# Kernel tuning notes

Measured on AMD Instinct MI355X. Metric: run time of the kernel, lower is better.

Reference implementation:

```python
import jax, jax.numpy as jnp
import numpy as np

N_GRAPHS = 64
NODES_PER_G = 640
N = N_GRAPHS * NODES_PER_G      # 40960 nodes
DEG = 16
E = N * DEG                     # 655360 edges
D = 128                         # hidden_dim == out_dim
POS = 16                        # pos_enc_dim
L = 4                           # n GatedGCN-LSPE layers
N_ATOM = 28
N_BOND = 4
EPS = 1e-6
BN_EPS = 1e-5


def _lin(x, w, b):
    return x @ w + b


def _bn(x, g, b):
    # torch BatchNorm1d training forward: biased batch stats
    m = x.mean(0)
    v = x.var(0)
    return (x - m) * jax.lax.rsqrt(v + BN_EPS) * g + b


def setup_inputs() -> dict:
    key = jax.random.key(0)
    ks = iter(jax.random.split(key, 64))
    def nrm(shape, s=0.1):
        return jax.random.normal(next(ks), shape, dtype=jnp.float32) * s
    h_atoms = jax.random.randint(next(ks), (N,), 0, N_ATOM)
    e_bonds = jax.random.randint(next(ks), (E,), 0, N_BOND)
    # keep edges within each graph of the batch
    epg = E // N_GRAPHS
    off = (jnp.arange(E) // epg) * NODES_PER_G
    src = jax.random.randint(next(ks), (E,), 0, NODES_PER_G) + off
    dst = jax.random.randint(next(ks), (E,), 0, NODES_PER_G) + off
    node_graph_ids = jnp.arange(N) // NODES_PER_G
    return dict(
        h_atoms=h_atoms, e_bonds=e_bonds, src=src, dst=dst,
        node_graph_ids=node_graph_ids,
        p=nrm((N, POS), 1.0),
        W_emb_h=nrm((N_ATOM, D)), W_emb_p=nrm((POS, D)), b_emb_p=nrm((D,)),
        W_emb_e=nrm((N_BOND, D)),
        A1_w=nrm((L, 2 * D, D)), A1_b=nrm((L, D)),
        A2_w=nrm((L, 2 * D, D)), A2_b=nrm((L, D)),
        B1_w=nrm((L, D, D)), B1_b=nrm((L, D)),
        B2_w=nrm((L, D, D)), B2_b=nrm((L, D)),
        B3_w=nrm((L, D, D)), B3_b=nrm((L, D)),
        C1_w=nrm((L, D, D)), C1_b=nrm((L, D)),
        C2_w=nrm((L, D, D)), C2_b=nrm((L, D)),
        bn_h_g=jnp.ones((L, D)), bn_h_b=jnp.zeros((L, D)),
        bn_e_g=jnp.ones((L, D)), bn_e_b=jnp.zeros((L, D)),
        p_out_w=nrm((D, POS)), p_out_b=nrm((POS,)),
        Whp_w=nrm((D + POS, D)), Whp_b=nrm((D,)),
        mlp_w0=nrm((D, D // 2)), mlp_b0=nrm((D // 2,)),
        mlp_w1=nrm((D // 2, D // 4)), mlp_b1=nrm((D // 4,)),
        mlp_w2=nrm((D // 4, 1)), mlp_b2=nrm((1,)),
    )


def _forward(p, W_emb_h, W_emb_p, b_emb_p, W_emb_e,
             A1_w, A1_b, A2_w, A2_b, B1_w, B1_b, B2_w, B2_b, B3_w, B3_b,
             C1_w, C1_b, C2_w, C2_b, bn_h_g, bn_h_b, bn_e_g, bn_e_b,
             p_out_w, p_out_b, Whp_w, Whp_b,
             mlp_w0, mlp_b0, mlp_w1, mlp_b1, mlp_w2, mlp_b2,
             h_atoms, e_bonds, src, dst, node_graph_ids):
    seg = lambda x, idx, n: jax.ops.segment_sum(x, idx, num_segments=n)
    h = W_emb_h[h_atoms]                      # [N,D] atom embedding
    pc = _lin(p, W_emb_p, b_emb_p)            # [N,D] PE embedding
    ef = W_emb_e[e_bonds]                     # [E,D] bond embedding
    for l in range(L):
        h_in, p_in, e_in = h, pc, ef
        # edge gates: hat_eta_ij = B1 h_i + B2 h_j + B3 e_ij (u=src, v=dst)
        hat_eta = (_lin(h, B1_w[l], B1_b[l])[src]
                   + _lin(h, B2_w[l], B2_b[l])[dst]
                   + _lin(ef, B3_w[l], B3_b[l]))          # [E,D]
        sig = jax.nn.sigmoid(hat_eta)
        eta = sig / (seg(sig, dst, N)[dst] + EPS)          # normalized gate
        hp = jnp.concatenate([h, pc], axis=-1)             # [N,2D]
        h_new = _lin(hp, A1_w[l], A1_b[l]) + seg(eta * _lin(hp, A2_w[l], A2_b[l])[src], dst, N)
        p_new = _lin(pc, C1_w[l], C1_b[l]) + seg(eta * _lin(pc, C2_w[l], C2_b[l])[src], dst, N)
        h_new = jax.nn.relu(_bn(h_new, bn_h_g[l], bn_h_b[l]))
        e_new = jax.nn.relu(_bn(hat_eta, bn_e_g[l], bn_e_b[l]))
        p_new = jnp.tanh(p_new)
        h = h_in + h_new       # residual (in_dim==out_dim)
        pc = p_in + p_new
        ef = e_in + e_new
    # pe_init == 'rand_walk' post-processing
    po = _lin(pc, p_out_w, p_out_b)                        # [N,POS]
    po = po - (seg(po, node_graph_ids, N_GRAPHS) / NODES_PER_G)[node_graph_ids]
    po = po / jnp.sqrt(seg(po * po, node_graph_ids, N_GRAPHS))[node_graph_ids]
    hp2 = _lin(jnp.concatenate([h, po], axis=-1), Whp_w, Whp_b)
    hg = seg(hp2, node_graph_ids, N_GRAPHS) / NODES_PER_G  # mean readout [G,D]
    y = jax.nn.relu(_lin(hg, mlp_w0, mlp_b0))
    y = jax.nn.relu(_lin(y, mlp_w1, mlp_b1))
    return _lin(y, mlp_w2, mlp_b2)                         # [G,1]


def reference(h_atoms, e_bonds, src, dst, node_graph_ids, p,
              W_emb_h, W_emb_p, b_emb_p, W_emb_e,
              A1_w, A1_b, A2_w, A2_b, B1_w, B1_b, B2_w, B2_b, B3_w, B3_b,
              C1_w, C1_b, C2_w, C2_b, bn_h_g, bn_h_b, bn_e_g, bn_e_b,
              p_out_w, p_out_b, Whp_w, Whp_b,
              mlp_w0, mlp_b0, mlp_w1, mlp_b1, mlp_w2, mlp_b2):
    return _forward(p, W_emb_h, W_emb_p, b_emb_p, W_emb_e,
                    A1_w, A1_b, A2_w, A2_b, B1_w, B1_b, B2_w, B2_b, B3_w, B3_b,
                    C1_w, C1_b, C2_w, C2_b, bn_h_g, bn_h_b, bn_e_g, bn_e_b,
                    p_out_w, p_out_b, Whp_w, Whp_b,
                    mlp_w0, mlp_b0, mlp_w1, mlp_b1, mlp_w2, mlp_b2,
                    h_atoms, e_bonds, src, dst, node_graph_ids)
```

## Files before the change

### kernel.cpp

```cpp
#include <hip/hip_runtime.h>
#include <math.h>

#define N_NODES 40960
#define N_EDGES 655360
#define NPG     640
#define NGRAPH  64
#define DH      128
#define NLAYERS 4
#define GATE_EPS 1e-6f
#define BN_EPS   1e-5f
#define ETPB    4

#define POOL_BYTES 580000000ull
__device__ __attribute__((aligned(256))) unsigned char g_pool[POOL_BYTES];

using short8  = __attribute__((ext_vector_type(8))) short;
using float4v = __attribute__((ext_vector_type(4))) float;

static __device__ __forceinline__ float sigmoidf_(float x) {
  return 1.f / (1.f + __expf(-x));
}
static __device__ __forceinline__ unsigned short f2bf(float f) {
  unsigned int u = __float_as_uint(f);
  unsigned int r = 0x7FFFu + ((u >> 16) & 1u);
  return (unsigned short)((u + r) >> 16);
}
static __device__ __forceinline__ float bf2f(unsigned short h) {
  return __uint_as_float(((unsigned int)h) << 16);
}

template <int WITH_STATS>
__global__ __launch_bounds__(256)
void egemm(const unsigned short* __restrict__ ef,
           const unsigned short* __restrict__ Wt,
           const float* __restrict__ bias,
           unsigned short* __restrict__ hat,
           const int* __restrict__ srcp, const int* __restrict__ dstp,
           const unsigned short* __restrict__ G1, const unsigned short* __restrict__ G2,
           float* __restrict__ stats, float* __restrict__ ssum)
{
  __shared__ unsigned short Ws[128][136];
  __shared__ float hatL[64][132];
  __shared__ int dstL[64];

  const int t    = threadIdx.x;
  const int w    = t >> 6;
  const int lane = t & 63;
  const int quad = lane >> 4;
  const int l16  = lane & 15;

#pragma unroll
  for (int i = 0; i < 8; ++i) {
    int flat = i * 256 + t;
    int n = flat >> 4, g = flat & 15;
    *reinterpret_cast<uint4*>(&Ws[n][g * 8]) =
        *reinterpret_cast<const uint4*>(&Wt[n * 128 + g * 8]);
  }
  __syncthreads();

  float stat_s = 0.f, stat_q = 0.f;

  for (int tile = 0; tile < ETPB; ++tile) {
    const size_t row0 = ((size_t)blockIdx.x * ETPB + tile) * 64;

    const size_t arow = row0 + w * 16 + l16;
    short8 a[4];
#pragma unroll
    for (int ks = 0; ks < 4; ++ks)
      a[ks] = *reinterpret_cast<const short8*>(&ef[arow * 128 + ks * 32 + quad * 8]);

    float4v acc[8];
#pragma unroll
    for (int j = 0; j < 8; ++j) acc[j] = (float4v){0.f, 0.f, 0.f, 0.f};
#pragma unroll
    for (int ks = 0; ks < 4; ++ks)
#pragma unroll
      for (int j = 0; j < 8; ++j) {
        short8 b = *reinterpret_cast<const short8*>(&Ws[j * 16 + l16][ks * 32 + quad * 8]);
        acc[j] = __builtin_amdgcn_mfma_f32_16x16x32_bf16(a[ks], b, acc[j], 0, 0, 0);
      }

    if (tile) __syncthreads();
#pragma unroll
    for (int j = 0; j < 8; ++j)
#pragma unroll
      for (int r = 0; r < 4; ++r)
        hatL[w * 16 + quad * 4 + r][j * 16 + l16] = acc[j][r];
    __syncthreads();

    {
      const int r = t >> 2, seg = t & 3;
      const size_t row = row0 + r;
      const int si = srcp[row], di = dstp[row];
      if (seg == 0) dstL[r] = di;
      const unsigned short* g1p = &G1[(size_t)si * 128];
      const unsigned short* g2p = &G2[(size_t)di * 128];
#pragma unroll
      for (int q2 = 0; q2 < 4; ++q2) {
        const int cc = seg * 32 + (((q2 + seg) & 3) << 3);
        float4 h0 = *reinterpret_cast<const float4*>(&hatL[r][cc]);
        float4 h1 = *reinterpret_cast<const float4*>(&hatL[r][cc + 4]);
        float4 b0 = *reinterpret_cast<const float4*>(&bias[cc]);
        float4 b1 = *reinterpret_cast<const float4*>(&bias[cc + 4]);
        uint4 g1 = *reinterpret_cast<const uint4*>(&g1p[cc]);
        uint4 g2 = *reinterpret_cast<const uint4*>(&g2p[cc]);
        float hv[8] = {h0.x, h0.y, h0.z, h0.w, h1.x, h1.y, h1.z, h1.w};
        float bv[8] = {b0.x, b0.y, b0.z, b0.w, b1.x, b1.y, b1.z, b1.w};
        unsigned int g1w[4] = {g1.x, g1.y, g1.z, g1.w};
        unsigned int g2w[4] = {g2.x, g2.y, g2.z, g2.w};
        unsigned int pk[4];
        float vr[8];
#pragma unroll
        for (int i = 0; i < 4; ++i) {
          float vlo = hv[2 * i]     + bv[2 * i]
                    + bf2f((unsigned short)(g1w[i] & 0xffffu))
                    + bf2f((unsigned short)(g2w[i] & 0xffffu));
          float vhi = hv[2 * i + 1] + bv[2 * i + 1]
                    + bf2f((unsigned short)(g1w[i] >> 16))
                    + bf2f((unsigned short)(g2w[i] >> 16));
          unsigned short lo = f2bf(vlo), hi = f2bf(vhi);
          pk[i] = (unsigned int)lo | ((unsigned int)hi << 16);
          vr[2 * i] = bf2f(lo); vr[2 * i + 1] = bf2f(hi);
        }
        uint4 st; st.x = pk[0]; st.y = pk[1]; st.z = pk[2]; st.w = pk[3];
        *reinterpret_cast<uint4*>(&hat[row * 128 + cc]) = st;
        float4 w0; w0.x = vr[0]; w0.y = vr[1]; w0.z = vr[2]; w0.w = vr[3];
        float4 w1; w1.x = vr[4]; w1.y = vr[5]; w1.z = vr[6]; w1.w = vr[7];
        *reinterpret_cast<float4*>(&hatL[r][cc])     = w0;
        *reinterpret_cast<float4*>(&hatL[r][cc + 4]) = w1;
      }
    }
    __syncthreads();

    if (WITH_STATS && t < 128) {
      float s = 0.f, q = 0.f;
#pragma unroll 8
      for (int r = 0; r < 64; ++r) {
        float v = hatL[r][t];
        s += v; q += v * v;
      }
      stat_s += s; stat_q += q;
    }
    if (t >= 128) {
      const int c = t - 128;
      float run = 0.f;
      int prev = dstL[0];
      for (int r = 0; r < 64; ++r) {
        int d = dstL[r];
        float sg = sigmoidf_(hatL[r][c]);
        if (d != prev) {
          atomicAdd(&ssum[(size_t)prev * 128 + c], run);
          run = 0.f; prev = d;
        }
        run += sg;
      }
      atomicAdd(&ssum[(size_t)prev * 128 + c], run);
    }
  }

  if (WITH_STATS && t < 128) {
    atomicAdd(&stats[t], stat_s);
    atomicAdd(&stats[128 + t], stat_q);
  }
}

__global__ __launch_bounds__(256)
void ngemm6(const unsigned short* __restrict__ hp,
            const unsigned short* __restrict__ WtL,
            const float* __restrict__ B1b, const float* __restrict__ B2b,
            const float* __restrict__ A1b, const float* __restrict__ A2b,
            const float* __restrict__ C1b, const float* __restrict__ C2b,
            unsigned short* __restrict__ B1h, unsigned short* __restrict__ B2h,
            float* __restrict__ A1hp, float* __restrict__ A2hp,
            float* __restrict__ C1p, float* __restrict__ C2p)
{
  __shared__ unsigned short As[64][264];

  const int t    = threadIdx.x;
  const int w    = t >> 6;
  const int lane = t & 63;
  const int quad = lane >> 4;
  const int l16  = lane & 15;
  const size_t row0 = (size_t)blockIdx.x * 64;

#pragma unroll
  for (int i = 0; i < 8; ++i) {
    int flat = i * 256 + t;
    int r = flat >> 5, g = flat & 31;
    *reinterpret_cast<uint4*>(&As[r][g * 8]) =
        *reinterpret_cast<const uint4*>(&hp[(row0 + r) * 256 + g * 8]);
  }
  __syncthreads();

  const unsigned short* Wm[6] = {WtL, WtL + 16384, WtL + 49152, WtL + 81920,
                                 WtL + 114688, WtL + 131072};
  const int Kk[6]   = {128, 128, 256, 256, 128, 128};
  const int koff[6] = {0, 0, 0, 0, 128, 128};
  const float* bs[6] = {B1b, B2b, A1b, A2b, C1b, C2b};
  float* outf[6] = {nullptr, nullptr, A1hp, A2hp, C1p, C2p};
  unsigned short* outb[2] = {B1h, B2h};

  for (int m = 0; m < 6; ++m) {
    const unsigned short* W = Wm[m];
    const int K = Kk[m], ko = koff[m];
    float4v acc[8];
#pragma unroll
    for (int j = 0; j < 8; ++j) acc[j] = (float4v){0.f, 0.f, 0.f, 0.f};
    for (int ks = 0; ks < K / 32; ++ks) {
      short8 a = *reinterpret_cast<const short8*>(&As[w * 16 + l16][ko + ks * 32 + quad * 8]);
#pragma unroll
      for (int j = 0; j < 8; ++j) {
        short8 b = *reinterpret_cast<const short8*>(&W[(size_t)(j * 16 + l16) * K + ks * 32 + quad * 8]);
        acc[j] = __builtin_amdgcn_mfma_f32_16x16x32_bf16(a, b, acc[j], 0, 0, 0);
      }
    }
    const float* bb = bs[m];
    if (m < 2) {
      unsigned short* o = outb[m];
#pragma unroll
      for (int j = 0; j < 8; ++j) {
        int col = j * 16 + l16;
        float bc = bb[col];
#pragma unroll
        for (int r = 0; r < 4; ++r) {
          size_t orow = row0 + w * 16 + quad * 4 + r;
          o[orow * 128 + col] = f2bf(acc[j][r] + bc);
        }
      }
    } else {
      float* o = outf[m];
#pragma unroll
      for (int j = 0; j < 8; ++j) {
        int col = j * 16 + l16;
        float bc = bb[col];
#pragma unroll
        for (int r = 0; r < 4; ++r) {
          size_t orow = row0 + w * 16 + quad * 4 + r;
          o[orow * 128 + col] = acc[j][r] + bc;
        }
      }
    }
  }
}

__global__ void prep_weights(const float* __restrict__ B1, const float* __restrict__ B2,
                             const float* __restrict__ B3, const float* __restrict__ A1,
                             const float* __restrict__ A2, const float* __restrict__ C1,
                             const float* __restrict__ C2, unsigned short* __restrict__ Wt)
{
  int idx = blockIdx.x * 256 + threadIdx.x;
  if (idx >= 4 * 147456) return;
  int layer = idx / 147456;
  int o = idx - layer * 147456;
  const float* src; int K, local;
  if (o < 16384)       { src = B1 + layer * 16384; local = o;          K = 128; }
  else if (o < 32768)  { src = B2 + layer * 16384; local = o - 16384;  K = 128; }
  else if (o < 49152)  { src = B3 + layer * 16384; local = o - 32768;  K = 128; }
  else if (o < 81920)  { src = A1 + layer * 32768; local = o - 49152;  K = 256; }
  else if (o < 114688) { src = A2 + layer * 32768; local = o - 81920;  K = 256; }
  else if (o < 131072) { src = C1 + layer * 16384; local = o - 114688; K = 128; }
  else                 { src = C2 + layer * 16384; local = o - 131072; K = 128; }
  int n = local / K, k = local - n * K;
  Wt[idx] = f2bf(src[k * 128 + n]);
}

__global__ void convert_hp(const float* __restrict__ h, const float* __restrict__ pc,
                           unsigned short* __restrict__ hp)
{
  int t = blockIdx.x * 256 + threadIdx.x;
  if (t >= N_NODES * 64) return;
  int n = t >> 6, part = t & 63;
  float4 v = (part < 32) ? reinterpret_cast<const float4*>(h)[n * 32 + part]
                         : reinterpret_cast<const float4*>(pc)[n * 32 + (part - 32)];
  ushort4 o;
  o.x = f2bf(v.x); o.y = f2bf(v.y); o.z = f2bf(v.z); o.w = f2bf(v.w);
  reinterpret_cast<ushort4*>(hp)[n * 64 + part] = o;
}

__global__ void embed_nodes_k(const int* __restrict__ idx, const float* __restrict__ table,
                              float* __restrict__ out, int M)
{
  int t = blockIdx.x * 256 + threadIdx.x;
  if (t < M * 32) {
    int r = t >> 5, c = t & 31;
    reinterpret_cast<float4*>(out)[t] =
        reinterpret_cast<const float4*>(table)[idx[r] * 32 + c];
  }
}

__global__ void embed_edges_bf(const int* __restrict__ bonds, const int* __restrict__ eidx,
                               const float* __restrict__ table,
                               unsigned short* __restrict__ out, int M)
{
  int t = blockIdx.x * 256 + threadIdx.x;
  if (t < M * 32) {
    int r = t >> 5, c = t & 31;
    float4 v = reinterpret_cast<const float4*>(table)[bonds[eidx[r]] * 32 + c];
    ushort4 o;
    o.x = f2bf(v.x); o.y = f2bf(v.y); o.z = f2bf(v.z); o.w = f2bf(v.w);
    reinterpret_cast<ushort4*>(out)[t] = o;
  }
}

__global__ void hist_k(const int* __restrict__ dstI, int* __restrict__ deg, int E)
{
  int e = blockIdx.x * 256 + threadIdx.x;
  if (e < E) atomicAdd(&deg[dstI[e]], 1);
}

__global__ void scan_k(const int* __restrict__ deg, int* __restrict__ row_start,
                       int* __restrict__ cursor, int n)
{
  __shared__ int buf[1024];
  __shared__ int carry;
  int t = threadIdx.x;
  if (t == 0) carry = 0;
  __syncthreads();
  for (int b0 = 0; b0 < n; b0 += 1024) {
    int v = (b0 + t < n) ? deg[b0 + t] : 0;
    buf[t] = v;
    __syncthreads();
    for (int off = 1; off < 1024; off <<= 1) {
      int add = (t >= off) ? buf[t - off] : 0;
      __syncthreads();
      buf[t] += add;
      __syncthreads();
    }
    int incl = buf[t];
    int excl = carry + incl - v;
    if (b0 + t < n) { row_start[b0 + t] = excl; cursor[b0 + t] = excl; }
    __syncthreads();
    if (t == 1023) carry += incl;
    __syncthreads();
  }
  if (t == 0) row_start[n] = carry;
}

__global__ void fill_k(const int* __restrict__ dstI, int* __restrict__ cursor,
                       int* __restrict__ eidx, int E)
{
  int e = blockIdx.x * 256 + threadIdx.x;
  if (e < E) {
    int p = atomicAdd(&cursor[dstI[e]], 1);
    eidx[p] = e;
  }
}

__global__ void permute_sd(const int* __restrict__ eidx, const int* __restrict__ srcI,
                           const int* __restrict__ dstI, int* __restrict__ srcp,
                           int* __restrict__ dstp, int E)
{
  int e = blockIdx.x * 256 + threadIdx.x;
  if (e < E) {
    int o = eidx[e];
    srcp[e] = srcI[o];
    dstp[e] = dstI[o];
  }
}

template <int EF_UPD>
__global__ __launch_bounds__(256)
void gate_agg5(const unsigned short* __restrict__ hat, const int* __restrict__ row_start,
               const int* __restrict__ srcp, const float* __restrict__ ssum,
               const float* __restrict__ A1hp, const float* __restrict__ A2hp,
               const float* __restrict__ C1p, const float* __restrict__ C2p,
               float* __restrict__ hraw, float* __restrict__ pc,
               unsigned short* __restrict__ ef, const float* __restrict__ ss_e,
               unsigned short* __restrict__ hp)
{
  int t = threadIdx.x;
  int node = blockIdx.x * 4 + (t >> 6);
  int lane = t & 63;
  int c = lane * 2;
  int beg = row_start[node], end = row_start[node + 1];

  float2 sv = *reinterpret_cast<const float2*>(&ssum[(size_t)node * 128 + c]);
  float inv0 = 1.f / (sv.x + GATE_EPS);
  float inv1 = 1.f / (sv.y + GATE_EPS);

  float2 eA, eB;
  if (EF_UPD) {
    eA = *reinterpret_cast<const float2*>(&ss_e[c]);
    eB = *reinterpret_cast<const float2*>(&ss_e[128 + c]);
  }

  float ha0 = 0.f, ha1 = 0.f, pa0 = 0.f, pa1 = 0.f;
  for (int e = beg; e < end; ++e) {
    int s = srcp[e];
    ushort2 hv = *reinterpret_cast<const ushort2*>(&hat[(size_t)e * 128 + c]);
    float hx = bf2f(hv.x), hy = bf2f(hv.y);
    float w0 = sigmoidf_(hx) * inv0;
    float w1 = sigmoidf_(hy) * inv1;
    float2 a2 = *reinterpret_cast<const float2*>(&A2hp[(size_t)s * 128 + c]);
    float2 c2 = *reinterpret_cast<const float2*>(&C2p[(size_t)s * 128 + c]);
    ha0 += w0 * a2.x; ha1 += w1 * a2.y;
    pa0 += w0 * c2.x; pa1 += w1 * c2.y;
    if (EF_UPD) {
      ushort2 ev = *reinterpret_cast<ushort2*>(&ef[(size_t)e * 128 + c]);
      float ex = bf2f(ev.x) + fmaxf(hx * eA.x + eB.x, 0.f);
      float ey = bf2f(ev.y) + fmaxf(hy * eA.y + eB.y, 0.f);
      ushort2 eo; eo.x = f2bf(ex); eo.y = f2bf(ey);
      *reinterpret_cast<ushort2*>(&ef[(size_t)e * 128 + c]) = eo;
    }
  }
  size_t ix = (size_t)node * 128 + c;
  float2 a1 = *reinterpret_cast<const float2*>(&A1hp[ix]);
  float2 c1 = *reinterpret_cast<const float2*>(&C1p[ix]);
  float2 hv; hv.x = a1.x + ha0; hv.y = a1.y + ha1;
  *reinterpret_cast<float2*>(&hraw[ix]) = hv;
  float2 pv = *reinterpret_cast<float2*>(&pc[ix]);
  pv.x += tanhf(c1.x + pa0);
  pv.y += tanhf(c1.y + pa1);
  *reinterpret_cast<float2*>(&pc[ix]) = pv;
  ushort2 ph; ph.x = f2bf(pv.x); ph.y = f2bf(pv.y);
  *reinterpret_cast<ushort2*>(&hp[(size_t)node * 256 + 128 + c]) = ph;
}

__global__ __launch_bounds__(128)
void col_stats(const float* __restrict__ x, float* __restrict__ stats, int rowsPerBlock)
{
  int d = threadIdx.x;
  size_t r0 = (size_t)blockIdx.x * rowsPerBlock;
  float s = 0.f, q = 0.f;
  for (int i = 0; i < rowsPerBlock; ++i) {
    float v = x[(r0 + i) * 128 + d];
    s += v; q += v * v;
  }
  atomicAdd(&stats[d], s);
  atomicAdd(&stats[128 + d], q);
}

__global__ void bn_finalize(const float* __restrict__ stats, const float* __restrict__ g,
                            const float* __restrict__ b, float invM, float* __restrict__ ss)
{
  int c = threadIdx.x;
  float m = stats[c] * invM;
  float v = stats[128 + c] * invM - m * m;
  float A = rsqrtf(v + BN_EPS) * g[c];
  ss[c] = A;
  ss[128 + c] = b[c] - m * A;
}

__global__ void apply_h(float* __restrict__ dest, const float* __restrict__ xraw,
                        const float* __restrict__ ss, unsigned short* __restrict__ hp,
                        int total4)
{
  int t = blockIdx.x * 256 + threadIdx.x;
  if (t >= total4) return;
  int c4 = t & 31, n = t >> 5;
  float4 x = reinterpret_cast<const float4*>(xraw)[t];
  float4 A = reinterpret_cast<const float4*>(ss)[c4];
  float4 B = reinterpret_cast<const float4*>(ss + 128)[c4];
  float4 dv = reinterpret_cast<float4*>(dest)[t];
  dv.x += fmaxf(x.x * A.x + B.x, 0.f);
  dv.y += fmaxf(x.y * A.y + B.y, 0.f);
  dv.z += fmaxf(x.z * A.z + B.z, 0.f);
  dv.w += fmaxf(x.w * A.w + B.w, 0.f);
  reinterpret_cast<float4*>(dest)[t] = dv;
  ushort4 o;
  o.x = f2bf(dv.x); o.y = f2bf(dv.y); o.z = f2bf(dv.z); o.w = f2bf(dv.w);
  *reinterpret_cast<ushort4*>(&hp[(size_t)n * 256 + c4 * 4]) = o;
}

template <int MODE>
__global__ __launch_bounds__(256)
void gemm_k(const float* __restrict__ Xa, int Ka,
            const float* __restrict__ Xb, int Kb,
            const float* __restrict__ W,
            const float* __restrict__ bias,
            float* __restrict__ out,
            float* __restrict__ hg, float inv_nodes, int npg)
{
  __shared__ float Xs[16][68];
  __shared__ float Ws[16][128];
  __shared__ float red[8][128];

  const int t  = threadIdx.x;
  const int ty = t >> 5;
  const int tx = t & 31;
  const int row0 = blockIdx.x * 64;
  const int K = Ka + Kb;

  float acc[8][4];
#pragma unroll
  for (int i = 0; i < 8; ++i)
#pragma unroll
    for (int j = 0; j < 4; ++j) acc[i][j] = 0.f;

  const int xr = t >> 2;
  const int xk = (t & 3) << 2;
  const int wr = t >> 5;
  const int wc = tx << 2;

  for (int kk = 0; kk < K; kk += 16) {
    const float* xbase; int ldk, kloc;
    if (kk < Ka) { xbase = Xa; ldk = Ka; kloc = kk; }
    else         { xbase = Xb; ldk = Kb; kloc = kk - Ka; }
    float4 xv = *reinterpret_cast<const float4*>(
        &xbase[(size_t)(row0 + xr) * ldk + kloc + xk]);
    Xs[xk + 0][xr] = xv.x; Xs[xk + 1][xr] = xv.y;
    Xs[xk + 2][xr] = xv.z; Xs[xk + 3][xr] = xv.w;

    float4 wv0 = *reinterpret_cast<const float4*>(&W[(size_t)(kk + wr) * 128 + wc]);
    float4 wv1 = *reinterpret_cast<const float4*>(&W[(size_t)(kk + wr + 8) * 128 + wc]);
    *reinterpret_cast<float4*>(&Ws[wr][wc])     = wv0;
    *reinterpret_cast<float4*>(&Ws[wr + 8][wc]) = wv1;
    __syncthreads();

#pragma unroll
    for (int k = 0; k < 16; ++k) {
      float4 b4 = *reinterpret_cast<const float4*>(&Ws[k][wc]);
      float4 a0 = *reinterpret_cast<const float4*>(&Xs[k][ty << 3]);
      float4 a1 = *reinterpret_cast<const float4*>(&Xs[k][(ty << 3) + 4]);
      float a[8] = {a0.x, a0.y, a0.z, a0.w, a1.x, a1.y, a1.z, a1.w};
      float b[4] = {b4.x, b4.y, b4.z, b4.w};
#pragma unroll
      for (int i = 0; i < 8; ++i) {
        acc[i][0] += a[i] * b[0];
        acc[i][1] += a[i] * b[1];
        acc[i][2] += a[i] * b[2];
        acc[i][3] += a[i] * b[3];
      }
    }
    __syncthreads();
  }

  float4 bb = *reinterpret_cast<const float4*>(&bias[wc]);
  float bv[4] = {bb.x, bb.y, bb.z, bb.w};

  if (MODE == 0) {
#pragma unroll
    for (int i = 0; i < 8; ++i) {
      int r = row0 + (ty << 3) + i;
      float4 ov;
      ov.x = acc[i][0] + bv[0]; ov.y = acc[i][1] + bv[1];
      ov.z = acc[i][2] + bv[2]; ov.w = acc[i][3] + bv[3];
      *reinterpret_cast<float4*>(&out[(size_t)r * 128 + wc]) = ov;
    }
  } else {
    float csum[4] = {0, 0, 0, 0};
#pragma unroll
    for (int i = 0; i < 8; ++i) {
      csum[0] += acc[i][0]; csum[1] += acc[i][1];
      csum[2] += acc[i][2]; csum[3] += acc[i][3];
    }
#pragma unroll
    for (int j = 0; j < 4; ++j) red[ty][wc + j] = csum[j];
    __syncthreads();
    if (ty == 0) {
      int g = row0 / npg;
#pragma unroll
      for (int j = 0; j < 4; ++j) {
        float s = 0;
#pragma unroll
        for (int q = 0; q < 8; ++q) s += red[q][wc + j];
        atomicAdd(&hg[(size_t)g * 128 + wc + j], (s + 64.f * bv[j]) * inv_nodes);
      }
    }
  }
}

__global__ __launch_bounds__(256)
void po_gemm(const float* __restrict__ pc, const float* __restrict__ w,
             const float* __restrict__ b, float* __restrict__ po)
{
  __shared__ float pcs[16][128];
  __shared__ float wl[128][16];
  int t = threadIdx.x;
  int n0 = blockIdx.x * 16;
  for (int i = t; i < 512; i += 256) {
    int r = i >> 5, c = (i & 31) << 2;
    *reinterpret_cast<float4*>(&pcs[r][c]) =
        *reinterpret_cast<const float4*>(&pc[(size_t)(n0 + r) * 128 + c]);
  }
  for (int i = t; i < 512; i += 256) {
    int r = i >> 2, c = (i & 3) << 2;
    *reinterpret_cast<float4*>(&wl[r][c]) =
        *reinterpret_cast<const float4*>(&w[r * 16 + c]);
  }
  __syncthreads();
  int i = t >> 4, j = t & 15;
  float acc = b[j];
  for (int k = 0; k < 128; ++k) acc += pcs[i][k] * wl[k][j];
  po[(size_t)(n0 + i) * 16 + j] = acc;
}

__global__ __launch_bounds__(256)
void pe_norm(float* __restrict__ po)
{
  int g = blockIdx.x;
  int t = threadIdx.x;
  int j = t & 15, grp = t >> 4;
  __shared__ float red[16][16];
  __shared__ float mean_s[16];
  __shared__ float nrm_s[16];
  size_t bse = (size_t)g * NPG * 16;
  float s = 0.f;
  for (int i = grp; i < NPG; i += 16) s += po[bse + i * 16 + j];
  red[grp][j] = s;
  __syncthreads();
  if (grp == 0) {
    float m = 0.f;
    for (int q = 0; q < 16; ++q) m += red[q][j];
    mean_s[j] = m / NPG;
  }
  __syncthreads();
  float m = mean_s[j];
  float q2 = 0.f;
  for (int i = grp; i < NPG; i += 16) {
    float c = po[bse + i * 16 + j] - m;
    q2 += c * c;
  }
  red[grp][j] = q2;
  __syncthreads();
  if (grp == 0) {
    float v = 0.f;
    for (int q = 0; q < 16; ++q) v += red[q][j];
    nrm_s[j] = sqrtf(v);
  }
  __syncthreads();
  float inv = 1.f / nrm_s[j];
  for (int i = grp; i < NPG; i += 16) {
    size_t ix = bse + i * 16 + j;
    po[ix] = (po[ix] - m) * inv;
  }
}

__global__ __launch_bounds__(256)
void mlp_head(const float* __restrict__ hg,
              const float* __restrict__ w0, const float* __restrict__ b0,
              const float* __restrict__ w1, const float* __restrict__ b1,
              const float* __restrict__ w2, const float* __restrict__ b2,
              float* __restrict__ out)
{
  __shared__ float hs[64 * 128];
  __shared__ float y0[64 * 64];
  __shared__ float y1[64 * 32];
  int t = threadIdx.x;
  for (int i = t; i < 64 * 128 / 4; i += 256)
    reinterpret_cast<float4*>(hs)[i] = reinterpret_cast<const float4*>(hg)[i];
  __syncthreads();
  for (int o = t; o < 64 * 64; o += 256) {
    int i = o >> 6, j = o & 63;
    float a = b0[j];
    for (int k = 0; k < 128; ++k) a += hs[i * 128 + k] * w0[k * 64 + j];
    y0[o] = fmaxf(a, 0.f);
  }
  __syncthreads();
  for (int o = t; o < 64 * 32; o += 256) {
    int i = o >> 5, j = o & 31;
    float a = b1[j];
    for (int k = 0; k < 64; ++k) a += y0[i * 64 + k] * w1[k * 32 + j];
    y1[o] = fmaxf(a, 0.f);
  }
  __syncthreads();
  if (t < 64) {
    float a = b2[0];
    for (int k = 0; k < 32; ++k) a += y1[t * 32 + k] * w2[k];
    out[t] = a;
  }
}

__global__ void fill_sentinel(float* out, int n, float v)
{
  int t = blockIdx.x * 256 + threadIdx.x;
  if (t < n) out[t] = v;
}

extern "C" void kernel_launch(void* const* d_in, const int* in_sizes, int n_in,
                              void* d_out, int out_size, void* d_ws, size_t ws_size,
                              hipStream_t stream)
{
  const int*   h_atoms = (const int*)d_in[0];
  const int*   e_bonds = (const int*)d_in[1];
  const int*   srcI    = (const int*)d_in[2];
  const int*   dstI    = (const int*)d_in[3];
  const float* p_in    = (const float*)d_in[5];
  const float* W_emb_h = (const float*)d_in[6];
  const float* W_emb_p = (const float*)d_in[7];
  const float* b_emb_p = (const float*)d_in[8];
  const float* W_emb_e = (const float*)d_in[9];
  const float* A1_w = (const float*)d_in[10];
  const float* A1_b = (const float*)d_in[11];
  const float* A2_w = (const float*)d_in[12];
  const float* A2_b = (const float*)d_in[13];
  const float* B1_w = (const float*)d_in[14];
  const float* B1_b = (const float*)d_in[15];
  const float* B2_w = (const float*)d_in[16];
  const float* B2_b = (const float*)d_in[17];
  const float* B3_w = (const float*)d_in[18];
  const float* B3_b = (const float*)d_in[19];
  const float* C1_w = (const float*)d_in[20];
  const float* C1_b = (const float*)d_in[21];
  const float* C2_w = (const float*)d_in[22];
  const float* C2_b = (const float*)d_in[23];
  const float* bn_h_g = (const float*)d_in[24];
  const float* bn_h_b = (const float*)d_in[25];
  const float* bn_e_g = (const float*)d_in[26];
  const float* bn_e_b = (const float*)d_in[27];
  const float* p_out_w = (const float*)d_in[28];
  const float* p_out_b = (const float*)d_in[29];
  const float* Whp_w   = (const float*)d_in[30];
  const float* Whp_b   = (const float*)d_in[31];
  const float* mlp_w0  = (const float*)d_in[32];
  const float* mlp_b0  = (const float*)d_in[33];
  const float* mlp_w1  = (const float*)d_in[34];
  const float* mlp_b1  = (const float*)d_in[35];
  const float* mlp_w2  = (const float*)d_in[36];
  const float* mlp_b2  = (const float*)d_in[37];

  static void* pool_ptr = nullptr;
  if (!pool_ptr) {
    if (hipGetSymbolAddress(&pool_ptr, HIP_SYMBOL(g_pool)) != hipSuccess || !pool_ptr) {
      fill_sentinel<<<dim3(1), dim3(256), 0, stream>>>((float*)d_out, out_size, 12345.0f);
      return;
    }
  }

  float* fbase = (float*)pool_ptr;
  size_t fo = 0;
  auto carvef = [&](size_t nf) { float* r = fbase + fo; fo += nf; return r; };
  float* h    = carvef((size_t)N_NODES * DH);
  float* pc   = carvef((size_t)N_NODES * DH);
  float* A1hp = carvef((size_t)N_NODES * DH);
  float* A2hp = carvef((size_t)N_NODES * DH);
  float* C1p  = carvef((size_t)N_NODES * DH);
  float* C2p  = carvef((size_t)N_NODES * DH);
  float* hraw = carvef((size_t)N_NODES * DH);
  float* ssum = carvef((size_t)N_NODES * DH);
  float* po   = carvef((size_t)N_NODES * 16);
  float* hg   = carvef(NGRAPH * 128);
  float* estats = carvef(256);
  float* hstats = carvef(256);
  float* ss_e   = carvef(256);
  float* ss_h   = carvef(256);

  unsigned short* ubase = (unsigned short*)(fbase + fo);
  unsigned short* ef_bf  = ubase;
  unsigned short* hat_bf = ef_bf + (size_t)N_EDGES * DH;
  unsigned short* hp_bf  = hat_bf + (size_t)N_EDGES * DH;
  unsigned short* b1_bf  = hp_bf + (size_t)N_NODES * 256;
  unsigned short* b2_bf  = b1_bf + (size_t)N_NODES * DH;
  unsigned short* Wt_bf  = b2_bf + (size_t)N_NODES * DH;
  int* ibase = (int*)(Wt_bf + 4 * 147456);
  int* deg       = ibase;
  int* row_start = deg + N_NODES;
  int* cursor    = row_start + (N_NODES + 3);
  int* eidx      = cursor + N_NODES;
  int* srcp      = eidx + N_EDGES;
  int* dstp      = srcp + N_EDGES;

  dim3 b256(256);

  prep_weights<<<dim3((4 * 147456 + 255) / 256), b256, 0, stream>>>(
      B1_w, B2_w, B3_w, A1_w, A2_w, C1_w, C2_w, Wt_bf);

  hipMemsetAsync(deg, 0, N_NODES * sizeof(int), stream);
  hist_k<<<dim3((N_EDGES + 255) / 256), b256, 0, stream>>>(dstI, deg, N_EDGES);
  scan_k<<<dim3(1), dim3(1024), 0, stream>>>(deg, row_start, cursor, N_NODES);
  fill_k<<<dim3((N_EDGES + 255) / 256), b256, 0, stream>>>(dstI, cursor, eidx, N_EDGES);
  permute_sd<<<dim3((N_EDGES + 255) / 256), b256, 0, stream>>>(eidx, srcI, dstI, srcp, dstp, N_EDGES);

  embed_nodes_k<<<dim3((N_NODES * 32 + 255) / 256), b256, 0, stream>>>(h_atoms, W_emb_h, h, N_NODES);
  embed_edges_bf<<<dim3((N_EDGES * 32 + 255) / 256), b256, 0, stream>>>(
      e_bonds, eidx, W_emb_e, ef_bf, N_EDGES);
  gemm_k<0><<<dim3(N_NODES / 64), b256, 0, stream>>>(
      p_in, 16, nullptr, 0, W_emb_p, b_emb_p, pc, nullptr, 0.f, NPG);
  convert_hp<<<dim3(N_NODES * 64 / 256), b256, 0, stream>>>(h, pc, hp_bf);

  const dim3 gNode64(N_NODES / 64), gEdge(N_EDGES / (64 * ETPB));

  for (int l = 0; l < NLAYERS; ++l) {
    const unsigned short* WtL = Wt_bf + (size_t)l * 147456;
    const unsigned short* WtB3 = WtL + 32768;
    const bool last = (l == NLAYERS - 1);

    ngemm6<<<gNode64, b256, 0, stream>>>(hp_bf, WtL,
        B1_b + l * 128, B2_b + l * 128, A1_b + l * 128, A2_b + l * 128,
        C1_b + l * 128, C2_b + l * 128, b1_bf, b2_bf, A1hp, A2hp, C1p, C2p);

    hipMemsetAsync(ssum, 0, (size_t)N_NODES * DH * sizeof(float), stream);
    if (!last) {
      hipMemsetAsync(estats, 0, 256 * sizeof(float), stream);
      egemm<1><<<gEdge, b256, 0, stream>>>(ef_bf, WtB3, B3_b + l * 128, hat_bf,
          srcp, dstp, b1_bf, b2_bf, estats, ssum);
      bn_finalize<<<dim3(1), dim3(128), 0, stream>>>(
          estats, bn_e_g + l * 128, bn_e_b + l * 128, 1.f / N_EDGES, ss_e);
      gate_agg5<1><<<dim3(N_NODES / 4), b256, 0, stream>>>(
          hat_bf, row_start, srcp, ssum, A1hp, A2hp, C1p, C2p, hraw, pc,
          ef_bf, ss_e, hp_bf);
    } else {
      egemm<0><<<gEdge, b256, 0, stream>>>(ef_bf, WtB3, B3_b + l * 128, hat_bf,
          srcp, dstp, b1_bf, b2_bf, nullptr, ssum);
      gate_agg5<0><<<dim3(N_NODES / 4), b256, 0, stream>>>(
          hat_bf, row_start, srcp, ssum, A1hp, A2hp, C1p, C2p, hraw, pc,
          nullptr, nullptr, hp_bf);
    }

    hipMemsetAsync(hstats, 0, 256 * sizeof(float), stream);
    col_stats<<<dim3(128), dim3(128), 0, stream>>>(hraw, hstats, N_NODES / 128);
    bn_finalize<<<dim3(1), dim3(128), 0, stream>>>(
        hstats, bn_h_g + l * 128, bn_h_b + l * 128, 1.f / N_NODES, ss_h);

    apply_h<<<dim3(N_NODES * 32 / 256), b256, 0, stream>>>(
        h, hraw, ss_h, hp_bf, N_NODES * 32);
  }

  po_gemm<<<dim3(N_NODES / 16), b256, 0, stream>>>(pc, p_out_w, p_out_b, po);
  pe_norm<<<dim3(NGRAPH), b256, 0, stream>>>(po);

  hipMemsetAsync(hg, 0, NGRAPH * 128 * sizeof(float), stream);
  gemm_k<2><<<dim3(N_NODES / 64), b256, 0, stream>>>(
      h, 128, po, 16, Whp_w, Whp_b, nullptr, hg, 1.f / NPG, NPG);

  mlp_head<<<dim3(1), b256, 0, stream>>>(
      hg, mlp_w0, mlp_b0, mlp_w1, mlp_b1, mlp_w2, mlp_b2, (float*)d_out);
}
```

Before: 3.068 ms.

## Pre-swizzle weights into MFMA fragment order and shrink gathered node features to bf16

```diff
diff --git a/kernel.cpp b/kernel.cpp
--- a/kernel.cpp
+++ b/kernel.cpp
@@ -39,8 +39,8 @@
            const unsigned short* __restrict__ G1, const unsigned short* __restrict__ G2,
            float* __restrict__ stats, float* __restrict__ ssum)
 {
-  __shared__ unsigned short Ws[128][136];
-  __shared__ float hatL[64][132];
+  __shared__ unsigned short Wl[16384];
+  __shared__ unsigned short hatB[64][136];
   __shared__ int dstL[64];
 
   const int t    = threadIdx.x;
@@ -48,21 +48,26 @@
   const int lane = t & 63;
   const int quad = lane >> 4;
   const int l16  = lane & 15;
-
-#pragma unroll
-  for (int i = 0; i < 8; ++i) {
-    int flat = i * 256 + t;
-    int n = flat >> 4, g = flat & 15;
-    *reinterpret_cast<uint4*>(&Ws[n][g * 8]) =
-        *reinterpret_cast<const uint4*>(&Wt[n * 128 + g * 8]);
-  }
+  const size_t base = (size_t)blockIdx.x * (64 * ETPB);
+  const int er = t >> 2;
+
+  int sI[ETPB], dI[ETPB];
+#pragma unroll
+  for (int tl = 0; tl < ETPB; ++tl) {
+    sI[tl] = srcp[base + tl * 64 + er];
+    dI[tl] = dstp[base + tl * 64 + er];
+  }
+
+#pragma unroll
+  for (int i = 0; i < 8; ++i)
+    *reinterpret_cast<uint4*>(&Wl[(i * 256 + t) * 8]) =
+        *reinterpret_cast<const uint4*>(&Wt[(i * 256 + t) * 8]);
   __syncthreads();
 
   float stat_s = 0.f, stat_q = 0.f;
 
   for (int tile = 0; tile < ETPB; ++tile) {
-    const size_t row0 = ((size_t)blockIdx.x * ETPB + tile) * 64;
-
+    const size_t row0 = base + tile * 64;
     const size_t arow = row0 + w * 16 + l16;
     short8 a[4];
 #pragma unroll
@@ -76,78 +81,83 @@
     for (int ks = 0; ks < 4; ++ks)
 #pragma unroll
       for (int j = 0; j < 8; ++j) {
-        short8 b = *reinterpret_cast<const short8*>(&Ws[j * 16 + l16][ks * 32 + quad * 8]);
+        short8 b = *reinterpret_cast<const short8*>(&Wl[((ks * 8 + j) * 64 + lane) * 8]);
         acc[j] = __builtin_amdgcn_mfma_f32_16x16x32_bf16(a[ks], b, acc[j], 0, 0, 0);
       }
 
     if (tile) __syncthreads();
-#pragma unroll
-    for (int j = 0; j < 8; ++j)
-#pragma unroll
-      for (int r = 0; r < 4; ++r)
-        hatL[w * 16 + quad * 4 + r][j * 16 + l16] = acc[j][r];
+    {
+      const int row = w * 16 + quad * 4;
+#pragma unroll
+      for (int j = 0; j < 8; ++j) {
+        const int chunk = (j * 16 + l16) >> 3;
+        const int off   = l16 & 7;
+#pragma unroll
+        for (int r = 0; r < 4; ++r) {
+          const int rr = row + r;
+          hatB[rr][((chunk ^ (rr & 15)) << 3) + off] = f2bf(acc[j][r]);
+        }
+      }
+    }
     __syncthreads();
 
     {
-      const int r = t >> 2, seg = t & 3;
+      const int r = er, seg = t & 3;
       const size_t row = row0 + r;
-      const int si = srcp[row], di = dstp[row];
+      const int si = sI[tile], di = dI[tile];
       if (seg == 0) dstL[r] = di;
       const unsigned short* g1p = &G1[(size_t)si * 128];
       const unsigned short* g2p = &G2[(size_t)di * 128];
+      const int key = r & 15;
 #pragma unroll
       for (int q2 = 0; q2 < 4; ++q2) {
-        const int cc = seg * 32 + (((q2 + seg) & 3) << 3);
-        float4 h0 = *reinterpret_cast<const float4*>(&hatL[r][cc]);
-        float4 h1 = *reinterpret_cast<const float4*>(&hatL[r][cc + 4]);
+        const int lch = seg * 4 + q2;
+        const int cc  = lch << 3;
+        const int pcc = (lch ^ key) << 3;
+        uint4 mm = *reinterpret_cast<const uint4*>(&hatB[r][pcc]);
         float4 b0 = *reinterpret_cast<const float4*>(&bias[cc]);
         float4 b1 = *reinterpret_cast<const float4*>(&bias[cc + 4]);
         uint4 g1 = *reinterpret_cast<const uint4*>(&g1p[cc]);
         uint4 g2 = *reinterpret_cast<const uint4*>(&g2p[cc]);
-        float hv[8] = {h0.x, h0.y, h0.z, h0.w, h1.x, h1.y, h1.z, h1.w};
-        float bv[8] = {b0.x, b0.y, b0.z, b0.w, b1.x, b1.y, b1.z, b1.w};
+        unsigned int mw[4] = {mm.x, mm.y, mm.z, mm.w};
         unsigned int g1w[4] = {g1.x, g1.y, g1.z, g1.w};
         unsigned int g2w[4] = {g2.x, g2.y, g2.z, g2.w};
+        float bv[8] = {b0.x, b0.y, b0.z, b0.w, b1.x, b1.y, b1.z, b1.w};
         unsigned int pk[4];
-        float vr[8];
 #pragma unroll
         for (int i = 0; i < 4; ++i) {
-          float vlo = hv[2 * i]     + bv[2 * i]
+          float vlo = bf2f((unsigned short)(mw[i] & 0xffffu)) + bv[2 * i]
                     + bf2f((unsigned short)(g1w[i] & 0xffffu))
                     + bf2f((unsigned short)(g2w[i] & 0xffffu));
-          float vhi = hv[2 * i + 1] + bv[2 * i + 1]
+          float vhi = bf2f((unsigned short)(mw[i] >> 16)) + bv[2 * i + 1]
                     + bf2f((unsigned short)(g1w[i] >> 16))
                     + bf2f((unsigned short)(g2w[i] >> 16));
-          unsigned short lo = f2bf(vlo), hi = f2bf(vhi);
-          pk[i] = (unsigned int)lo | ((unsigned int)hi << 16);
-          vr[2 * i] = bf2f(lo); vr[2 * i + 1] = bf2f(hi);
+          pk[i] = (unsigned int)f2bf(vlo) | ((unsigned int)f2bf(vhi) << 16);
         }
         uint4 st; st.x = pk[0]; st.y = pk[1]; st.z = pk[2]; st.w = pk[3];
         *reinterpret_cast<uint4*>(&hat[row * 128 + cc]) = st;
-        float4 w0; w0.x = vr[0]; w0.y = vr[1]; w0.z = vr[2]; w0.w = vr[3];
-        float4 w1; w1.x = vr[4]; w1.y = vr[5]; w1.z = vr[6]; w1.w = vr[7];
-        *reinterpret_cast<float4*>(&hatL[r][cc])     = w0;
-        *reinterpret_cast<float4*>(&hatL[r][cc + 4]) = w1;
+        *reinterpret_cast<uint4*>(&hatB[r][pcc]) = st;
       }
     }
     __syncthreads();
 
     if (WITH_STATS && t < 128) {
+      const int ch = t >> 3, off = t & 7;
       float s = 0.f, q = 0.f;
 #pragma unroll 8
       for (int r = 0; r < 64; ++r) {
-        float v = hatL[r][t];
+        float v = bf2f(hatB[r][((ch ^ (r & 15)) << 3) + off]);
         s += v; q += v * v;
       }
       stat_s += s; stat_q += q;
     }
     if (t >= 128) {
-      const int c = t - 128;
+      const int c = t - 128, ch = c >> 3, off = c & 7;
       float run = 0.f;
       int prev = dstL[0];
       for (int r = 0; r < 64; ++r) {
         int d = dstL[r];
-        float sg = sigmoidf_(hatL[r][c]);
+        float sg = sigmoidf_(bf2f(hatB[r][((ch ^ (r & 15)) << 3) + off]));
         if (d != prev) {
           atomicAdd(&ssum[(size_t)prev * 128 + c], run);
           run = 0.f; prev = d;
@@ -171,8 +181,8 @@
             const float* __restrict__ A1b, const float* __restrict__ A2b,
             const float* __restrict__ C1b, const float* __restrict__ C2b,
             unsigned short* __restrict__ B1h, unsigned short* __restrict__ B2h,
-            float* __restrict__ A1hp, float* __restrict__ A2hp,
-            float* __restrict__ C1p, float* __restrict__ C2p)
+            float* __restrict__ A1hp, unsigned short* __restrict__ a2_bf,
+            float* __restrict__ C1p, unsigned short* __restrict__ c2_bf)
 {
   __shared__ unsigned short As[64][264];
 
@@ -197,8 +207,8 @@
   const int Kk[6]   = {128, 128, 256, 256, 128, 128};
   const int koff[6] = {0, 0, 0, 0, 128, 128};
   const float* bs[6] = {B1b, B2b, A1b, A2b, C1b, C2b};
-  float* outf[6] = {nullptr, nullptr, A1hp, A2hp, C1p, C2p};
-  unsigned short* outb[2] = {B1h, B2h};
+  float* outf[6] = {nullptr, nullptr, A1hp, nullptr, C1p, nullptr};
+  unsigned short* outb[6] = {B1h, B2h, nullptr, a2_bf, nullptr, c2_bf};
 
   for (int m = 0; m < 6; ++m) {
     const unsigned short* W = Wm[m];
@@ -207,15 +217,15 @@
 #pragma unroll
     for (int j = 0; j < 8; ++j) acc[j] = (float4v){0.f, 0.f, 0.f, 0.f};
     for (int ks = 0; ks < K / 32; ++ks) {
-      short8 a = *reinterpret_cast<const short8*>(&As[w * 16 + l16][ko + ks * 32 + quad * 8]);
+      short8 aa = *reinterpret_cast<const short8*>(&As[w * 16 + l16][ko + ks * 32 + quad * 8]);
 #pragma unroll
       for (int j = 0; j < 8; ++j) {
-        short8 b = *reinterpret_cast<const short8*>(&W[(size_t)(j * 16 + l16) * K + ks * 32 + quad * 8]);
-        acc[j] = __builtin_amdgcn_mfma_f32_16x16x32_bf16(a, b, acc[j], 0, 0, 0);
+        short8 b = *reinterpret_cast<const short8*>(&W[((ks * 8 + j) * 64 + lane) * 8]);
+        acc[j] = __builtin_amdgcn_mfma_f32_16x16x32_bf16(aa, b, acc[j], 0, 0, 0);
       }
     }
     const float* bb = bs[m];
-    if (m < 2) {
+    if (outb[m]) {
       unsigned short* o = outb[m];
 #pragma unroll
       for (int j = 0; j < 8; ++j) {
@@ -252,15 +262,20 @@
   if (idx >= 4 * 147456) return;
   int layer = idx / 147456;
   int o = idx - layer * 147456;
-  const float* src; int K, local;
-  if (o < 16384)       { src = B1 + layer * 16384; local = o;          K = 128; }
-  else if (o < 32768)  { src = B2 + layer * 16384; local = o - 16384;  K = 128; }
-  else if (o < 49152)  { src = B3 + layer * 16384; local = o - 32768;  K = 128; }
-  else if (o < 81920)  { src = A1 + layer * 32768; local = o - 49152;  K = 256; }
-  else if (o < 114688) { src = A2 + layer * 32768; local = o - 81920;  K = 256; }
-  else if (o < 131072) { src = C1 + layer * 16384; local = o - 114688; K = 128; }
-  else                 { src = C2 + layer * 16384; local = o - 131072; K = 128; }
-  int n = local / K, k = local - n * K;
+  const float* src; int local;
+  if (o < 16384)       { src = B1 + layer * 16384; local = o;          }
+  else if (o < 32768)  { src = B2 + layer * 16384; local = o - 16384;  }
+  else if (o < 49152)  { src = B3 + layer * 16384; local = o - 32768;  }
+  else if (o < 81920)  { src = A1 + layer * 32768; local = o - 49152;  }
+  else if (o < 114688) { src = A2 + layer * 32768; local = o - 81920;  }
+  else if (o < 131072) { src = C1 + layer * 16384; local = o - 114688; }
+  else                 { src = C2 + layer * 16384; local = o - 131072; }
+  int i    = local & 7;
+  int lane = (local >> 3) & 63;
+  int fj   = local >> 9;
+  int j    = fj & 7, ks = fj >> 3;
+  int n = j * 16 + (lane & 15);
+  int k = ks * 32 + (lane >> 4) * 8 + i;
   Wt[idx] = f2bf(src[k * 128 + n]);
 }
 
@@ -362,8 +377,8 @@
 __global__ __launch_bounds__(256)
 void gate_agg5(const unsigned short* __restrict__ hat, const int* __restrict__ row_start,
                const int* __restrict__ srcp, const float* __restrict__ ssum,
-               const float* __restrict__ A1hp, const float* __restrict__ A2hp,
-               const float* __restrict__ C1p, const float* __restrict__ C2p,
+               const float* __restrict__ A1hp, const unsigned short* __restrict__ a2_bf,
+               const float* __restrict__ C1p, const unsigned short* __restrict__ c2_bf,
                float* __restrict__ hraw, float* __restrict__ pc,
                unsigned short* __restrict__ ef, const float* __restrict__ ss_e,
                unsigned short* __restrict__ hp)
@@ -385,22 +400,27 @@
   }
 
   float ha0 = 0.f, ha1 = 0.f, pa0 = 0.f, pa1 = 0.f;
-  for (int e = beg; e < end; ++e) {
-    int s = srcp[e];
-    ushort2 hv = *reinterpret_cast<const ushort2*>(&hat[(size_t)e * 128 + c]);
-    float hx = bf2f(hv.x), hy = bf2f(hv.y);
-    float w0 = sigmoidf_(hx) * inv0;
-    float w1 = sigmoidf_(hy) * inv1;
-    float2 a2 = *reinterpret_cast<const float2*>(&A2hp[(size_t)s * 128 + c]);
-    float2 c2 = *reinterpret_cast<const float2*>(&C2p[(size_t)s * 128 + c]);
-    ha0 += w0 * a2.x; ha1 += w1 * a2.y;
-    pa0 += w0 * c2.x; pa1 += w1 * c2.y;
-    if (EF_UPD) {
-      ushort2 ev = *reinterpret_cast<ushort2*>(&ef[(size_t)e * 128 + c]);
-      float ex = bf2f(ev.x) + fmaxf(hx * eA.x + eB.x, 0.f);
-      float ey = bf2f(ev.y) + fmaxf(hy * eA.y + eB.y, 0.f);
-      ushort2 eo; eo.x = f2bf(ex); eo.y = f2bf(ey);
-      *reinterpret_cast<ushort2*>(&ef[(size_t)e * 128 + c]) = eo;
+  for (int b0 = beg; b0 < end; b0 += 64) {
+    int nb = min(64, end - b0);
+    int sreg = (b0 + lane < end) ? srcp[b0 + lane] : 0;
+    for (int k = 0; k < nb; ++k) {
+      int e = b0 + k;
+      int s = __shfl(sreg, k);
+      ushort2 hv = *reinterpret_cast<const ushort2*>(&hat[(size_t)e * 128 + c]);
+      float hx = bf2f(hv.x), hy = bf2f(hv.y);
+      float w0 = sigmoidf_(hx) * inv0;
+      float w1 = sigmoidf_(hy) * inv1;
+      ushort2 a2 = *reinterpret_cast<const ushort2*>(&a2_bf[(size_t)s * 128 + c]);
+      ushort2 c2 = *reinterpret_cast<const ushort2*>(&c2_bf[(size_t)s * 128 + c]);
+      ha0 += w0 * bf2f(a2.x); ha1 += w1 * bf2f(a2.y);
+      pa0 += w0 * bf2f(c2.x); pa1 += w1 * bf2f(c2.y);
+      if (EF_UPD) {
+        ushort2 ev = *reinterpret_cast<ushort2*>(&ef[(size_t)e * 128 + c]);
+        float ex = bf2f(ev.x) + fmaxf(hx * eA.x + eB.x, 0.f);
+        float ey = bf2f(ev.y) + fmaxf(hy * eA.y + eB.y, 0.f);
+        ushort2 eo; eo.x = f2bf(ex); eo.y = f2bf(ey);
+        *reinterpret_cast<ushort2*>(&ef[(size_t)e * 128 + c]) = eo;
+      }
     }
   }
   size_t ix = (size_t)node * 128 + c;
@@ -723,9 +743,7 @@
   float* h    = carvef((size_t)N_NODES * DH);
   float* pc   = carvef((size_t)N_NODES * DH);
   float* A1hp = carvef((size_t)N_NODES * DH);
-  float* A2hp = carvef((size_t)N_NODES * DH);
   float* C1p  = carvef((size_t)N_NODES * DH);
-  float* C2p  = carvef((size_t)N_NODES * DH);
   float* hraw = carvef((size_t)N_NODES * DH);
   float* ssum = carvef((size_t)N_NODES * DH);
   float* po   = carvef((size_t)N_NODES * 16);
@@ -741,7 +759,9 @@
   unsigned short* hp_bf  = hat_bf + (size_t)N_EDGES * DH;
   unsigned short* b1_bf  = hp_bf + (size_t)N_NODES * 256;
   unsigned short* b2_bf  = b1_bf + (size_t)N_NODES * DH;
-  unsigned short* Wt_bf  = b2_bf + (size_t)N_NODES * DH;
+  unsigned short* a2_bf  = b2_bf + (size_t)N_NODES * DH;
+  unsigned short* c2_bf  = a2_bf + (size_t)N_NODES * DH;
+  unsigned short* Wt_bf  = c2_bf + (size_t)N_NODES * DH;
   int* ibase = (int*)(Wt_bf + 4 * 147456);
   int* deg       = ibase;
   int* row_start = deg + N_NODES;
@@ -777,7 +797,7 @@
 
     ngemm6<<<gNode64, b256, 0, stream>>>(hp_bf, WtL,
         B1_b + l * 128, B2_b + l * 128, A1_b + l * 128, A2_b + l * 128,
-        C1_b + l * 128, C2_b + l * 128, b1_bf, b2_bf, A1hp, A2hp, C1p, C2p);
+        C1_b + l * 128, C2_b + l * 128, b1_bf, b2_bf, A1hp, a2_bf, C1p, c2_bf);
 
     hipMemsetAsync(ssum, 0, (size_t)N_NODES * DH * sizeof(float), stream);
     if (!last) {
@@ -787,13 +807,13 @@
       bn_finalize<<<dim3(1), dim3(128), 0, stream>>>(
           estats, bn_e_g + l * 128, bn_e_b + l * 128, 1.f / N_EDGES, ss_e);
       gate_agg5<1><<<dim3(N_NODES / 4), b256, 0, stream>>>(
-          hat_bf, row_start, srcp, ssum, A1hp, A2hp, C1p, C2p, hraw, pc,
+          hat_bf, row_start, srcp, ssum, A1hp, a2_bf, C1p, c2_bf, hraw, pc,
           ef_bf, ss_e, hp_bf);
     } else {
       egemm<0><<<gEdge, b256, 0, stream>>>(ef_bf, WtB3, B3_b + l * 128, hat_bf,
           srcp, dstp, b1_bf, b2_bf, nullptr, ssum);
       gate_agg5<0><<<dim3(N_NODES / 4), b256, 0, stream>>>(
-          hat_bf, row_start, srcp, ssum, A1hp, A2hp, C1p, C2p, hraw, pc,
+          hat_bf, row_start, srcp, ssum, A1hp, a2_bf, C1p, c2_bf, hraw, pc,
           nullptr, nullptr, hp_bf);
     }
 
```

New measurement: 3.250 ms. 1.06x slower.
